# Kernel tuning notes

Hardware: AMD Instinct MI355X
Metric: run time of the kernel (lower is better)

## Reference

```python
import jax, jax.numpy as jnp
import numpy as np
from jax import lax

NUM_LAYERS = 4
D_MODEL = 768
D_STATE = 128
D_CONV = 4
EXPAND = 2
HEADDIM = 64
D_INNER = EXPAND * D_MODEL            # 1536
NHEADS = D_INNER // HEADDIM           # 24
NGROUPS = 1
CONV_DIM = D_INNER + 2 * NGROUPS * D_STATE        # 1792 (x, B, C go through conv)
D_PROJ = 2 * D_INNER + 2 * NGROUPS * D_STATE + NHEADS  # z, xBC, dt
BATCH, SEQ = 4, 2048


def silu(x):
    return x * jax.nn.sigmoid(x)


def rmsnorm(x, w, eps):
    xf = x.astype(jnp.float32)
    var = jnp.mean(xf * xf, axis=-1, keepdims=True)
    return (w * (xf * lax.rsqrt(var + eps)).astype(x.dtype))


def ssd_scan(xh, dt, A, B, C):
    # xh: (b,s,h,p)  dt: (b,s,h)  A: (h,)  B,C: (b,s,n)
    b = xh.shape[0]
    dA = jnp.exp(dt * A)  # (b,s,h)
    # time-major for scan
    dA_s = dA.transpose(1, 0, 2)          # (s,b,h)
    dt_s = dt.transpose(1, 0, 2)          # (s,b,h)
    x_s = xh.transpose(1, 0, 2, 3)        # (s,b,h,p)
    B_s = B.transpose(1, 0, 2)            # (s,b,n)
    C_s = C.transpose(1, 0, 2)            # (s,b,n)

    h0 = jnp.zeros((b, NHEADS, HEADDIM, D_STATE), xh.dtype)

    def step(h, inp):
        dA_t, dt_t, x_t, B_t, C_t = inp
        # h_t = exp(dt*A) * h_{t-1} + dt * x outer B
        dBx = (dt_t[:, :, None, None] * x_t[:, :, :, None]) * B_t[:, None, None, :]
        h = dA_t[:, :, None, None] * h + dBx
        y = jnp.einsum('bhpn,bn->bhp', h, C_t)
        return h, y

    _, ys = lax.scan(step, h0, (dA_s, dt_s, x_s, B_s, C_s))
    return ys.transpose(1, 0, 2, 3)  # (b,s,h,p)


def mamba2_block(x, Wi, cw, cb, dtb, Alog, Dp, gw, Wo):
    b, s, _ = x.shape
    zxbcdt = jnp.einsum('bsd,ed->bse', x, Wi)  # (b,s,D_PROJ)
    z = zxbcdt[..., :D_INNER]
    xBC = zxbcdt[..., D_INNER:D_INNER + CONV_DIM]
    dt = zxbcdt[..., D_INNER + CONV_DIM:]

    # causal depthwise conv over time on (x,B,C)
    xc = xBC.transpose(0, 2, 1)  # (b, conv_dim, s)
    xc = lax.conv_general_dilated(xc, cw[:, None, :], (1,), [(D_CONV - 1, 0)],
                                  feature_group_count=CONV_DIM)
    xc = xc + cb[None, :, None]
    xBC = silu(xc.transpose(0, 2, 1))

    x_ssm = xBC[..., :D_INNER]
    Bm = xBC[..., D_INNER:D_INNER + D_STATE]
    Cm = xBC[..., D_INNER + D_STATE:]

    dt = jax.nn.softplus(dt + dtb)           # (b,s,h)
    A = -jnp.exp(Alog)                       # (h,)
    xh = x_ssm.reshape(b, s, NHEADS, HEADDIM)

    y = ssd_scan(xh, dt, A, Bm, Cm) + Dp[None, None, :, None] * xh
    y = y.reshape(b, s, D_INNER)
    y = y * silu(z)                          # gated
    y = rmsnorm(y, gw, 1e-5)
    return jnp.einsum('bse,de->bsd', y, Wo)


def setup_inputs() -> dict:
    key = jax.random.key(0)
    ks = jax.random.split(key, 12)
    L = NUM_LAYERS
    sc_in = 1.0 / np.sqrt(D_MODEL)
    sc_out = 1.0 / np.sqrt(D_INNER)
    sc_conv = np.sqrt(2.0 / D_CONV)
    u = jax.random.uniform(ks[5], (L, NHEADS), minval=1e-3, maxval=0.1)
    return {
        'x': jax.random.normal(ks[0], (BATCH, SEQ, D_MODEL), jnp.float32),
        'in_proj_w': jax.random.normal(ks[1], (L, D_PROJ, D_MODEL), jnp.float32) * sc_in,
        'conv_w': jax.random.normal(ks[2], (L, CONV_DIM, D_CONV), jnp.float32) * sc_conv,
        'conv_b': jnp.zeros((L, CONV_DIM), jnp.float32),
        'dt_bias': jnp.log(jnp.expm1(u)),
        'A_log': jnp.log(jax.random.uniform(ks[6], (L, NHEADS), minval=1.0, maxval=16.0)),
        'D_skip': jnp.ones((L, NHEADS), jnp.float32),
        'gnorm_w': jnp.ones((L, D_INNER), jnp.float32),
        'out_proj_w': jax.random.normal(ks[7], (L, D_MODEL, D_INNER), jnp.float32) * sc_out,
        'ln_w': jnp.ones((L, D_MODEL), jnp.float32),
        'final_ln_w': jnp.ones((D_MODEL,), jnp.float32),
    }


def reference(x, in_proj_w, conv_w, conv_b, dt_bias, A_log, D_skip, gnorm_w,
              out_proj_w, ln_w, final_ln_w):
    for l in range(NUM_LAYERS):
        residual = x
        h = rmsnorm(x, ln_w[l], 1e-6)
        h = mamba2_block(h, in_proj_w[l], conv_w[l], conv_b[l], dt_bias[l],
                         A_log[l], D_skip[l], gnorm_w[l], out_proj_w[l])
        x = h + residual
    return rmsnorm(x, final_ln_w, 1e-6)
```

## Files before the change

kernel.cpp:

```cpp
#include <hip/hip_runtime.h>
#include <hip/hip_bf16.h>
#include <math.h>

#define NUM_LAYERS 4
#define D_MODEL 768
#define D_STATE 128
#define D_CONV 4
#define HEADDIM 64
#define D_INNER 1536
#define NHEADS 24
#define CONV_DIM 1792
#define D_PROJ 3352
#define BATCH 4
#define SEQ 2048
#define NROWS (BATCH*SEQ)
#define CHUNK 128
#define NCHUNK (SEQ/CHUNK)
#define LOG2E 1.4426950408889634f

typedef __bf16 bf16x8 __attribute__((ext_vector_type(8)));
typedef float f32x4 __attribute__((ext_vector_type(4)));

#define GLL(gsrc, ldst)                                                        \
  __builtin_amdgcn_global_load_lds(                                            \
      (const __attribute__((address_space(1))) unsigned int*)(gsrc),           \
      (__attribute__((address_space(3))) unsigned int*)(ldst), 16, 0, 0)

__device__ __forceinline__ float warp_reduce_sum(float v) {
  v += __shfl_xor(v, 32);
  v += __shfl_xor(v, 16);
  v += __shfl_xor(v, 8);
  v += __shfl_xor(v, 4);
  v += __shfl_xor(v, 2);
  v += __shfl_xor(v, 1);
  return v;
}

__device__ __forceinline__ float softplusf(float x) {
  return (x > 20.f) ? x : log1pf(expf(x));
}
__device__ __forceinline__ float siluf(float x) {
  return x / (1.f + expf(-x));
}

__device__ __forceinline__ void store_val(float v, float* p) { *p = v; }
__device__ __forceinline__ void store_val(float v, __hip_bfloat16* p) {
  *p = __float2bfloat16(v);
}

__global__ __launch_bounds__(256) void f32_to_bf16_kernel(
    const float* __restrict__ in, __hip_bfloat16* __restrict__ out, size_t n) {
  for (size_t i = ((size_t)blockIdx.x * 256 + threadIdx.x) * 4; i < n;
       i += (size_t)gridDim.x * 256 * 4) {
    float4 v = *(const float4*)(in + i);
    __hip_bfloat16 h0 = __float2bfloat16(v.x), h1 = __float2bfloat16(v.y);
    __hip_bfloat16 h2 = __float2bfloat16(v.z), h3 = __float2bfloat16(v.w);
    ushort4 u;
    u.x = *(unsigned short*)&h0; u.y = *(unsigned short*)&h1;
    u.z = *(unsigned short*)&h2; u.w = *(unsigned short*)&h3;
    *(ushort4*)(out + i) = u;
  }
}

template <typename OUT>
__global__ __launch_bounds__(256) void rmsnorm768_kernel(
    const float* __restrict__ in, const float* __restrict__ w,
    OUT* __restrict__ out, float eps) {
  int row = blockIdx.x;
  const float* x = in + (size_t)row * D_MODEL;
  OUT* o = out + (size_t)row * D_MODEL;
  int t = threadIdx.x;
  float v0 = x[t], v1 = x[t + 256], v2 = x[t + 512];
  float ss = v0 * v0 + v1 * v1 + v2 * v2;
  __shared__ float sred[4];
  ss = warp_reduce_sum(ss);
  if ((t & 63) == 0) sred[t >> 6] = ss;
  __syncthreads();
  float tot = sred[0] + sred[1] + sred[2] + sred[3];
  float inv = rsqrtf(tot / (float)D_MODEL + eps);
  store_val(w[t] * v0 * inv, o + t);
  store_val(w[t + 256] * v1 * inv, o + t + 256);
  store_val(w[t + 512] * v2 * inv, o + t + 512);
}

#define GEMM_PROLOGUE_AND_MAINLOOP(Asrc, Wsrc, Kdim)                           \
  int t = threadIdx.x;                                                         \
  int w = t >> 6, l = t & 63;                                                  \
  int NT = (Kdim) >> 5;                                                        \
  int ldsA0 = (w * 64) * 8;                                                    \
  int ldsA1 = (256 + w * 64) * 8;                                              \
  int lr = l & 15, lk = l >> 4;                                                \
  int wr = w >> 1, wc = w & 1;                                                 \
  int aoff = (lk * 128 + wr * 64 + lr) * 8;                                    \
  int boff = (lk * 128 + wc * 64 + lr) * 8;                                    \
  f32x4 acc[4][4];                                                             \
  _Pragma("unroll") for (int i = 0; i < 4; i++)                                \
      _Pragma("unroll") for (int j = 0; j < 4; j++) acc[i][j] = (f32x4)0.f;    \
  STAGE(0, 0);                                                                 \
  for (int kt = 0; kt < NT; ++kt) {                                            \
    int cur = kt & 1;                                                          \
    if (kt + 1 < NT) {                                                         \
      STAGE(cur ^ 1, (kt + 1) * 32);                                           \
      asm volatile("s_waitcnt vmcnt(4)" ::: "memory");                         \
    } else {                                                                   \
      asm volatile("s_waitcnt vmcnt(0)" ::: "memory");                         \
    }                                                                          \
    __builtin_amdgcn_sched_barrier(0);                                         \
    __builtin_amdgcn_s_barrier();                                              \
    __builtin_amdgcn_sched_barrier(0);                                         \
    bf16x8 av[4], bv[4];                                                       \
    _Pragma("unroll") for (int mi = 0; mi < 4; mi++)                           \
        av[mi] = *(const bf16x8*)&At[cur][aoff + mi * 128];                    \
    _Pragma("unroll") for (int ni = 0; ni < 4; ni++)                           \
        bv[ni] = *(const bf16x8*)&Bt[cur][boff + ni * 128];                    \
    _Pragma("unroll") for (int mi = 0; mi < 4; mi++)                           \
        _Pragma("unroll") for (int ni = 0; ni < 4; ni++)                       \
            acc[mi][ni] = __builtin_amdgcn_mfma_f32_16x16x32_bf16(             \
                av[mi], bv[ni], acc[mi][ni], 0, 0, 0);                         \
    __builtin_amdgcn_sched_barrier(0);                                         \
    __builtin_amdgcn_s_barrier();                                              \
  }

#define STAGE(buf, kofs)                                                       \
  do {                                                                         \
    GLL(Aptr + (kofs), &At[buf][ldsA0]);                                       \
    GLL(Aptr + (kofs) + 16, &At[buf][ldsA1]);                                  \
    GLL(Wptr + (kofs), &Bt[buf][ldsA0]);                                       \
    GLL(Wptr + (kofs) + 16, &Bt[buf][ldsA1]);                                  \
  } while (0)

__global__ __launch_bounds__(256) void gemm_bf16_kernel(
    const __hip_bfloat16* __restrict__ A, const __hip_bfloat16* __restrict__ W,
    const float* __restrict__ res, float* __restrict__ C,
    int M, int N, int K) {
  __shared__ __bf16 At[2][4096];
  __shared__ __bf16 Bt[2][4096];
  int cpx = gridDim.x >> 3;
  int bid = blockIdx.x;
  int bid2 = (bid & 7) * cpx + (bid >> 3);
  int nbn = (N + 127) >> 7;
  int bn = bid2 % nbn;
  int bm = bid2 / nbn;
  int m0 = bm * 128, n0 = bn * 128;
  int srow = threadIdx.x & 127;
  int kbase = (threadIdx.x >> 7) * 8;
  const __hip_bfloat16* Aptr = A + (size_t)(m0 + srow) * K + kbase;
  int nrow = n0 + srow; if (nrow >= N) nrow = N - 1;
  const __hip_bfloat16* Wptr = W + (size_t)nrow * K + kbase;

  GEMM_PROLOGUE_AND_MAINLOOP(A, W, K)

  int rbase = (l >> 4) * 4;
#pragma unroll
  for (int ni = 0; ni < 4; ni++) {
    int n = n0 + wc * 64 + ni * 16 + (l & 15);
    if (n >= N) continue;
#pragma unroll
    for (int mi = 0; mi < 4; mi++) {
#pragma unroll
      for (int r = 0; r < 4; r++) {
        int m = m0 + wr * 64 + mi * 16 + rbase + r;
        float v = acc[mi][ni][r];
        if (res) v += res[(size_t)m * N + n];
        C[(size_t)m * N + n] = v;
      }
    }
  }
}

__global__ __launch_bounds__(256) void gemm_inproj_kernel(
    const __hip_bfloat16* __restrict__ A, const __hip_bfloat16* __restrict__ W,
    __hip_bfloat16* __restrict__ zout, __hip_bfloat16* __restrict__ xout,
    float* __restrict__ dtout) {
  const int K = D_MODEL, N = D_PROJ;
  __shared__ __bf16 At[2][4096];
  __shared__ __bf16 Bt[2][4096];
  int cpx = gridDim.x >> 3;
  int bid = blockIdx.x;
  int bid2 = (bid & 7) * cpx + (bid >> 3);
  int bn = bid2 % 27;
  int bm = bid2 / 27;
  int m0 = bm * 128, n0 = bn * 128;
  int srow = threadIdx.x & 127;
  int kbase = (threadIdx.x >> 7) * 8;
  const __hip_bfloat16* Aptr = A + (size_t)(m0 + srow) * K + kbase;
  int nrow = n0 + srow; if (nrow >= N) nrow = N - 1;
  const __hip_bfloat16* Wptr = W + (size_t)nrow * K + kbase;

  GEMM_PROLOGUE_AND_MAINLOOP(A, W, K)

  int rbase = (l >> 4) * 4;
  if (bn < 12) {
#pragma unroll
    for (int ni = 0; ni < 4; ni++) {
      int n = n0 + wc * 64 + ni * 16 + (l & 15);
#pragma unroll
      for (int mi = 0; mi < 4; mi++)
#pragma unroll
        for (int r = 0; r < 4; r++) {
          int m = m0 + wr * 64 + mi * 16 + rbase + r;
          zout[(size_t)m * D_INNER + n] = __float2bfloat16(acc[mi][ni][r]);
        }
    }
  } else if (bn < 26) {
    int nb = n0 - D_INNER;
#pragma unroll
    for (int ni = 0; ni < 4; ni++) {
      int n = nb + wc * 64 + ni * 16 + (l & 15);
#pragma unroll
      for (int mi = 0; mi < 4; mi++)
#pragma unroll
        for (int r = 0; r < 4; r++) {
          int m = m0 + wr * 64 + mi * 16 + rbase + r;
          xout[(size_t)m * CONV_DIM + n] = __float2bfloat16(acc[mi][ni][r]);
        }
    }
  } else {
#pragma unroll
    for (int ni = 0; ni < 4; ni++) {
      int col = wc * 64 + ni * 16 + (l & 15);
      if (col >= 24) continue;
#pragma unroll
      for (int mi = 0; mi < 4; mi++)
#pragma unroll
        for (int r = 0; r < 4; r++) {
          int m = m0 + wr * 64 + mi * 16 + rbase + r;
          dtout[(size_t)m * 24 + col] = acc[mi][ni][r];
        }
    }
  }
}

__global__ __launch_bounds__(128) void dt_kernel(
    const float* __restrict__ dtraw, const float* __restrict__ dt_bias,
    const float* __restrict__ A_log, float* __restrict__ dtbuf,
    float* __restrict__ cum2buf) {
  int c = blockIdx.x & 15;
  int h = (blockIdx.x >> 4) % NHEADS;
  int b = blockIdx.x / (16 * NHEADS);
  int t = threadIdx.x;
  int s = c * CHUNK + t;
  float Ah = -expf(A_log[h]);
  float raw = dtraw[((size_t)b * SEQ + s) * 24 + h] + dt_bias[h];
  float dt = softplusf(raw);
  __shared__ float sc[128];
  sc[t] = dt * Ah;
  __syncthreads();
  for (int off = 1; off < 128; off <<= 1) {
    float v = (t >= off) ? sc[t - off] : 0.f;
    __syncthreads();
    sc[t] += v;
    __syncthreads();
  }
  size_t o = ((size_t)b * NHEADS + h) * SEQ + s;
  dtbuf[o] = dt;
  cum2buf[o] = sc[t] * LOG2E;
}

__global__ __launch_bounds__(256) void conv_tiles_kernel(
    const __hip_bfloat16* __restrict__ xbc, const float* __restrict__ cw,
    const float* __restrict__ cb, __hip_bfloat16* __restrict__ xA,
    __hip_bfloat16* __restrict__ Bkt, __hip_bfloat16* __restrict__ Bkn,
    __hip_bfloat16* __restrict__ Ckn) {
  __shared__ float srows[11 * CONV_DIM];
  int to = blockIdx.x & 15;
  int c  = (blockIdx.x >> 4) & 15;
  int b  = blockIdx.x >> 8;
  int t  = threadIdx.x;
  int sb = c * CHUNK + to * 8;
  const __hip_bfloat16* base = xbc + (size_t)b * SEQ * CONV_DIM;
  for (int e = t; e < 11 * 224; e += 256) {
    int r = e / 224, c8 = (e - r * 224) * 8;
    int s = sb - 3 + r;
    float* dst = &srows[r * CONV_DIM + c8];
    if (s >= 0) {
      bf16x8 v = *(const bf16x8*)&base[(size_t)s * CONV_DIM + c8];
#pragma unroll
      for (int j = 0; j < 8; j++) dst[j] = (float)v[j];
    } else {
#pragma unroll
      for (int j = 0; j < 8; j++) dst[j] = 0.f;
    }
  }
  __syncthreads();
  int bc = b * 16 + c;
#pragma unroll
  for (int k7 = 0; k7 < 7; k7++) {
    int ch = t + k7 * 256;
    float w0 = cw[ch * 4], w1 = cw[ch * 4 + 1];
    float w2 = cw[ch * 4 + 2], w3 = cw[ch * 4 + 3];
    float bias = cb[ch];
    float out[8];
#pragma unroll
    for (int j = 0; j < 8; j++) {
      float a = bias;
      a = fmaf(srows[(j + 0) * CONV_DIM + ch], w0, a);
      a = fmaf(srows[(j + 1) * CONV_DIM + ch], w1, a);
      a = fmaf(srows[(j + 2) * CONV_DIM + ch], w2, a);
      a = fmaf(srows[(j + 3) * CONV_DIM + ch], w3, a);
      out[j] = siluf(a);
    }
    if (ch < D_INNER) {
      int h = ch >> 6, p = ch & 63;
      bf16x8 v;
#pragma unroll
      for (int j = 0; j < 8; j++) v[j] = (__bf16)out[j];
      *(bf16x8*)&xA[((((size_t)bc * 24 + h) * 16 + to) * 64 + p) * 8] = v;
    } else if (ch < D_INNER + D_STATE) {
      int n = ch - D_INNER;
      bf16x8 v;
#pragma unroll
      for (int j = 0; j < 8; j++) v[j] = (__bf16)out[j];
      *(bf16x8*)&Bkt[(((size_t)bc * 16 + to) * 128 + n) * 8] = v;
      __hip_bfloat16* dst = Bkn + (size_t)bc * 16384 + ((n >> 3) * 128) * 8 + (n & 7);
#pragma unroll
      for (int j = 0; j < 8; j++)
        dst[(to * 8 + j) * 8] = __float2bfloat16(out[j]);
    } else {
      int n = ch - D_INNER - D_STATE;
      __hip_bfloat16* dst = Ckn + (size_t)bc * 16384 + ((n >> 3) * 128) * 8 + (n & 7);
#pragma unroll
      for (int j = 0; j < 8; j++)
        dst[(to * 8 + j) * 8] = __float2bfloat16(out[j]);
    }
  }
}

__global__ __launch_bounds__(256) void ssd_state_kernel(
    const __hip_bfloat16* __restrict__ xA, const __hip_bfloat16* __restrict__ Bkt,
    const float* __restrict__ dtbuf, const float* __restrict__ cum2buf,
    __hip_bfloat16* __restrict__ states) {
  __shared__ __bf16 sX[8192];
  __shared__ __bf16 sB[16384];
  __shared__ float swdt[128];
  int c = blockIdx.x & 15;
  int h = (blockIdx.x >> 4) % NHEADS;
  int b = blockIdx.x / (16 * NHEADS);
  int t = threadIdx.x;
  int l = t & 63, w = t >> 6;
  const __hip_bfloat16* xsrc = xA + ((size_t)(b * 16 + c) * 24 + h) * 8192;
  const __hip_bfloat16* bsrc = Bkt + (size_t)(b * 16 + c) * 16384;
#pragma unroll
  for (int i = 0; i < 4; i++) GLL(xsrc + (i * 256 + t) * 8, &sX[(i * 256 + t) * 8]);
#pragma unroll
  for (int i = 0; i < 8; i++) GLL(bsrc + (i * 256 + t) * 8, &sB[(i * 256 + t) * 8]);
  {
    size_t dto = ((size_t)b * NHEADS + h) * SEQ + c * CHUNK;
    if (t < 128) {
      float total2 = cum2buf[dto + 127];
      swdt[t] = dtbuf[dto + t] * exp2f(total2 - cum2buf[dto + t]);
    }
  }
  __syncthreads();
#pragma unroll
  for (int i = 0; i < 4; i++) {
    int o = i * 256 + t;
    int to = o >> 6;
    bf16x8 v = *(bf16x8*)&sX[o * 8];
#pragma unroll
    for (int j = 0; j < 8; j++)
      v[j] = (__bf16)((float)v[j] * swdt[to * 8 + j]);
    *(bf16x8*)&sX[o * 8] = v;
  }
  __syncthreads();
  int n0w = w * 32;
  f32x4 acc[4][2];
#pragma unroll
  for (int i = 0; i < 4; i++)
#pragma unroll
    for (int j = 0; j < 2; j++) acc[i][j] = (f32x4)0.f;
#pragma unroll
  for (int kk = 0; kk < 4; kk++) {
    int ko = kk * 4 + (l >> 4);
    bf16x8 av[4], bv[2];
#pragma unroll
    for (int mi = 0; mi < 4; mi++)
      av[mi] = *(const bf16x8*)&sX[(ko * 64 + mi * 16 + (l & 15)) * 8];
#pragma unroll
    for (int ni = 0; ni < 2; ni++)
      bv[ni] = *(const bf16x8*)&sB[(ko * 128 + n0w + ni * 16 + (l & 15)) * 8];
#pragma unroll
    for (int mi = 0; mi < 4; mi++)
#pragma unroll
      for (int ni = 0; ni < 2; ni++)
        acc[mi][ni] = __builtin_amdgcn_mfma_f32_16x16x32_bf16(
            av[mi], bv[ni], acc[mi][ni], 0, 0, 0);
  }
  __hip_bfloat16* dst = states + (((size_t)b * NHEADS + h) * 16 + c) * 8192;
#pragma unroll
  for (int mi = 0; mi < 4; mi++)
#pragma unroll
    for (int ni = 0; ni < 2; ni++) {
      int n = n0w + ni * 16 + (l & 15);
#pragma unroll
      for (int r = 0; r < 4; r++) {
        int p = mi * 16 + (l >> 4) * 4 + r;
        dst[((n >> 3) * 64 + p) * 8 + (n & 7)] = __float2bfloat16(acc[mi][ni][r]);
      }
    }
}

__global__ __launch_bounds__(256) void ssd_chunkscan_kernel(
    __hip_bfloat16* __restrict__ states, const float* __restrict__ cum2buf) {
  int q = blockIdx.x & 3;
  int bh = blockIdx.x >> 2;
  int t = threadIdx.x;
  int o = q * 256 + t;
  __hip_bfloat16* base = states + (size_t)bh * NCHUNK * 8192 + (size_t)o * 8;
  const float* c2 = cum2buf + (size_t)bh * SEQ;
  float hacc[8];
#pragma unroll
  for (int j = 0; j < 8; j++) hacc[j] = 0.f;
  for (int c = 0; c < NCHUNK; c++) {
    float eA = exp2f(c2[c * 128 + 127]);
    __hip_bfloat16* p = base + (size_t)c * 8192;
    bf16x8 v = *(bf16x8*)p;
    bf16x8 wv;
#pragma unroll
    for (int j = 0; j < 8; j++) {
      float tmp = (float)v[j];
      wv[j] = (__bf16)hacc[j];
      hacc[j] = fmaf(eA, hacc[j], tmp);
    }
    *(bf16x8*)p = wv;
  }
}

__global__ __launch_bounds__(256) void ssd_output_kernel(
    const __hip_bfloat16* __restrict__ Ckn, const __hip_bfloat16* __restrict__ Bkn,
    const __hip_bfloat16* __restrict__ xA, const __hip_bfloat16* __restrict__ states,
    const float* __restrict__ dtbuf, const float* __restrict__ cum2buf,
    const float* __restrict__ D_skip, __hip_bfloat16* __restrict__ y) {
  __shared__ __bf16 sC[16384];
  __shared__ __bf16 sBS[16384];
  __shared__ __bf16 sXH[8192];
  int c = blockIdx.x & 15;
  int h = (blockIdx.x >> 4) % NHEADS;
  int b = blockIdx.x / (16 * NHEADS);
  int t = threadIdx.x;
  int l = t & 63, w = t >> 6;
  int bc = b * 16 + c;
  const __hip_bfloat16* csrc = Ckn + (size_t)bc * 16384;
  const __hip_bfloat16* bsrc = Bkn + (size_t)bc * 16384;
  const __hip_bfloat16* xsrc = xA + ((size_t)bc * 24 + h) * 8192;
#pragma unroll
  for (int i = 0; i < 8; i++) GLL(csrc + (i * 256 + t) * 8, &sC[(i * 256 + t) * 8]);
#pragma unroll
  for (int i = 0; i < 8; i++) GLL(bsrc + (i * 256 + t) * 8, &sBS[(i * 256 + t) * 8]);
#pragma unroll
  for (int i = 0; i < 4; i++) GLL(xsrc + (i * 256 + t) * 8, &sXH[(i * 256 + t) * 8]);

  size_t dto = ((size_t)b * NHEADS + h) * SEQ + c * CHUNK;
  float cum2_t[8], cum2_tau[8], dt_tau[8];
#pragma unroll
  for (int fm = 0; fm < 2; fm++)
#pragma unroll
    for (int r = 0; r < 4; r++)
      cum2_t[fm * 4 + r] = cum2buf[dto + w * 32 + fm * 16 + (l >> 4) * 4 + r];
#pragma unroll
  for (int fc = 0; fc < 8; fc++) {
    cum2_tau[fc] = cum2buf[dto + fc * 16 + (l & 15)];
    dt_tau[fc] = dtbuf[dto + fc * 16 + (l & 15)];
  }
  float Dh = D_skip[h];
  __syncthreads();

  f32x4 g[2][8];
#pragma unroll
  for (int i = 0; i < 2; i++)
#pragma unroll
    for (int j = 0; j < 8; j++) g[i][j] = (f32x4)0.f;
#pragma unroll
  for (int kk = 0; kk < 4; kk++) {
    int ko = kk * 4 + (l >> 4);
    bf16x8 a0 = *(const bf16x8*)&sC[(ko * 128 + w * 32 + (l & 15)) * 8];
    bf16x8 a1 = *(const bf16x8*)&sC[(ko * 128 + w * 32 + 16 + (l & 15)) * 8];
#pragma unroll
    for (int fc = 0; fc < 8; fc++) {
      bf16x8 bv = *(const bf16x8*)&sBS[(ko * 128 + fc * 16 + (l & 15)) * 8];
      g[0][fc] = __builtin_amdgcn_mfma_f32_16x16x32_bf16(a0, bv, g[0][fc], 0, 0, 0);
      g[1][fc] = __builtin_amdgcn_mfma_f32_16x16x32_bf16(a1, bv, g[1][fc], 0, 0, 0);
    }
  }
  __syncthreads();

#pragma unroll
  for (int fm = 0; fm < 2; fm++)
#pragma unroll
    for (int fc = 0; fc < 8; fc++) {
      int tau = fc * 16 + (l & 15);
#pragma unroll
      for (int r = 0; r < 4; r++) {
        int tt = w * 32 + fm * 16 + (l >> 4) * 4 + r;
        float v = 0.f;
        if (tt >= tau) {
          v = exp2f(cum2_t[fm * 4 + r] - cum2_tau[fc]) * dt_tau[fc] * g[fm][fc][r];
          if (tt == tau) v += Dh;
        }
        sBS[((tau >> 3) * 128 + tt) * 8 + (tau & 7)] = (__bf16)v;
      }
    }
  f32x4 y1[2][4];
#pragma unroll
  for (int i = 0; i < 2; i++)
#pragma unroll
    for (int j = 0; j < 4; j++) y1[i][j] = (f32x4)0.f;
#pragma unroll
  for (int kk = 0; kk < 4; kk++) {
    int ko = kk * 4 + (l >> 4);
    bf16x8 a0 = *(const bf16x8*)&sBS[(ko * 128 + w * 32 + (l & 15)) * 8];
    bf16x8 a1 = *(const bf16x8*)&sBS[(ko * 128 + w * 32 + 16 + (l & 15)) * 8];
#pragma unroll
    for (int fc = 0; fc < 4; fc++) {
      bf16x8 bv = *(const bf16x8*)&sXH[(ko * 64 + fc * 16 + (l & 15)) * 8];
      y1[0][fc] = __builtin_amdgcn_mfma_f32_16x16x32_bf16(a0, bv, y1[0][fc], 0, 0, 0);
      y1[1][fc] = __builtin_amdgcn_mfma_f32_16x16x32_bf16(a1, bv, y1[1][fc], 0, 0, 0);
    }
  }
  __syncthreads();
  const __hip_bfloat16* hsrc = states + (((size_t)b * NHEADS + h) * 16 + c) * 8192;
#pragma unroll
  for (int i = 0; i < 4; i++) GLL(hsrc + (i * 256 + t) * 8, &sXH[(i * 256 + t) * 8]);
  __syncthreads();

  f32x4 y2[2][4];
#pragma unroll
  for (int i = 0; i < 2; i++)
#pragma unroll
    for (int j = 0; j < 4; j++) y2[i][j] = (f32x4)0.f;
#pragma unroll
  for (int kk = 0; kk < 4; kk++) {
    int ko = kk * 4 + (l >> 4);
    bf16x8 a0 = *(const bf16x8*)&sC[(ko * 128 + w * 32 + (l & 15)) * 8];
    bf16x8 a1 = *(const bf16x8*)&sC[(ko * 128 + w * 32 + 16 + (l & 15)) * 8];
#pragma unroll
    for (int fc = 0; fc < 4; fc++) {
      bf16x8 bv = *(const bf16x8*)&sXH[(ko * 64 + fc * 16 + (l & 15)) * 8];
      y2[0][fc] = __builtin_amdgcn_mfma_f32_16x16x32_bf16(a0, bv, y2[0][fc], 0, 0, 0);
      y2[1][fc] = __builtin_amdgcn_mfma_f32_16x16x32_bf16(a1, bv, y2[1][fc], 0, 0, 0);
    }
  }

  __hip_bfloat16* yr = y + ((size_t)b * SEQ + c * CHUNK) * D_INNER + h * 64;
#pragma unroll
  for (int fm = 0; fm < 2; fm++)
#pragma unroll
    for (int r = 0; r < 4; r++) {
      int tt = w * 32 + fm * 16 + (l >> 4) * 4 + r;
      float sdec = exp2f(cum2_t[fm * 4 + r]);
#pragma unroll
      for (int fc = 0; fc < 4; fc++) {
        int p = fc * 16 + (l & 15);
        yr[(size_t)tt * D_INNER + p] =
            __float2bfloat16(y1[fm][fc][r] + sdec * y2[fm][fc][r]);
      }
    }
}

__global__ __launch_bounds__(192) void gate_norm_kernel(
    __hip_bfloat16* __restrict__ y, const __hip_bfloat16* __restrict__ z,
    const float* __restrict__ gw) {
  int row = blockIdx.x;
  const __hip_bfloat16* zr = z + (size_t)row * D_INNER;
  __hip_bfloat16* yr = y + (size_t)row * D_INNER;
  int t = threadIdx.x;
  bf16x8 yv = *(const bf16x8*)&yr[t * 8];
  bf16x8 zv = *(const bf16x8*)&zr[t * 8];
  float vals[8];
  float ss = 0.f;
#pragma unroll
  for (int j = 0; j < 8; j++) {
    float zf = (float)zv[j];
    float v = (float)yv[j] * siluf(zf);
    vals[j] = v;
    ss += v * v;
  }
  __shared__ float sred[3];
  ss = warp_reduce_sum(ss);
  if ((t & 63) == 0) sred[t >> 6] = ss;
  __syncthreads();
  float tot = sred[0] + sred[1] + sred[2];
  float inv = rsqrtf(tot / (float)D_INNER + 1e-5f);
  bf16x8 o;
#pragma unroll
  for (int j = 0; j < 8; j++)
    o[j] = (__bf16)(gw[t * 8 + j] * vals[j] * inv);
  *(bf16x8*)&yr[t * 8] = o;
}

extern "C" void kernel_launch(void* const* d_in, const int* in_sizes, int n_in,
                              void* d_out, int out_size, void* d_ws, size_t ws_size,
                              hipStream_t stream) {
  const float* x          = (const float*)d_in[0];
  const float* in_proj_w  = (const float*)d_in[1];
  const float* conv_w     = (const float*)d_in[2];
  const float* conv_b     = (const float*)d_in[3];
  const float* dt_bias    = (const float*)d_in[4];
  const float* A_log      = (const float*)d_in[5];
  const float* D_skip     = (const float*)d_in[6];
  const float* gnorm_w    = (const float*)d_in[7];
  const float* out_proj_w = (const float*)d_in[8];
  const float* ln_w       = (const float*)d_in[9];
  const float* final_ln_w = (const float*)d_in[10];

  float* ws = (float*)d_ws;
  float* curx   = ws; ws += (size_t)NROWS * D_MODEL;
  float* dtraw  = ws; ws += (size_t)NROWS * 24;
  float* dtbuf  = ws; ws += (size_t)BATCH * NHEADS * SEQ;
  float* cum2   = ws; ws += (size_t)BATCH * NHEADS * SEQ;
  __hip_bfloat16* zbuf   = (__hip_bfloat16*)ws; ws += (size_t)NROWS * D_INNER / 2;
  __hip_bfloat16* xbcbuf = (__hip_bfloat16*)ws; ws += (size_t)NROWS * CONV_DIM / 2;
  __hip_bfloat16* hbuf_b = (__hip_bfloat16*)ws; ws += (size_t)NROWS * D_MODEL / 2;
  __hip_bfloat16* ybuf_b = (__hip_bfloat16*)ws; ws += (size_t)NROWS * D_INNER / 2;
  __hip_bfloat16* wi_b   = (__hip_bfloat16*)ws; ws += (size_t)NUM_LAYERS * D_PROJ * D_MODEL / 2;
  __hip_bfloat16* wo_b   = (__hip_bfloat16*)ws; ws += (size_t)NUM_LAYERS * D_MODEL * D_INNER / 2;
  __hip_bfloat16* xAb    = (__hip_bfloat16*)ws; ws += (size_t)BATCH * NCHUNK * 24 * 8192 / 2;
  __hip_bfloat16* Bkt    = (__hip_bfloat16*)ws; ws += (size_t)BATCH * NCHUNK * 16384 / 2;
  __hip_bfloat16* Bkn    = (__hip_bfloat16*)ws; ws += (size_t)BATCH * NCHUNK * 16384 / 2;
  __hip_bfloat16* Ckn    = (__hip_bfloat16*)ws; ws += (size_t)BATCH * NCHUNK * 16384 / 2;
  __hip_bfloat16* states = (__hip_bfloat16*)ws;

  f32_to_bf16_kernel<<<1024, 256, 0, stream>>>(
      in_proj_w, wi_b, (size_t)NUM_LAYERS * D_PROJ * D_MODEL);
  f32_to_bf16_kernel<<<1024, 256, 0, stream>>>(
      out_proj_w, wo_b, (size_t)NUM_LAYERS * D_MODEL * D_INNER);

  for (int l = 0; l < NUM_LAYERS; l++) {
    const float* xin = (l == 0) ? x : curx;
    rmsnorm768_kernel<__hip_bfloat16><<<NROWS, 256, 0, stream>>>(
        xin, ln_w + (size_t)l * D_MODEL, hbuf_b, 1e-6f);

    gemm_inproj_kernel<<<64 * 27, 256, 0, stream>>>(
        hbuf_b, wi_b + (size_t)l * D_PROJ * D_MODEL, zbuf, xbcbuf, dtraw);

    dt_kernel<<<BATCH * NHEADS * NCHUNK, 128, 0, stream>>>(
        dtraw, dt_bias + l * NHEADS, A_log + l * NHEADS, dtbuf, cum2);

    conv_tiles_kernel<<<BATCH * NCHUNK * 16, 256, 0, stream>>>(
        xbcbuf, conv_w + (size_t)l * CONV_DIM * D_CONV,
        conv_b + (size_t)l * CONV_DIM, xAb, Bkt, Bkn, Ckn);

    ssd_state_kernel<<<BATCH * NHEADS * NCHUNK, 256, 0, stream>>>(
        xAb, Bkt, dtbuf, cum2, states);

    ssd_chunkscan_kernel<<<BATCH * NHEADS * 4, 256, 0, stream>>>(states, cum2);

    ssd_output_kernel<<<BATCH * NHEADS * NCHUNK, 256, 0, stream>>>(
        Ckn, Bkn, xAb, states, dtbuf, cum2, D_skip + l * NHEADS, ybuf_b);

    gate_norm_kernel<<<NROWS, 192, 0, stream>>>(
        ybuf_b, zbuf, gnorm_w + (size_t)l * D_INNER);

    gemm_bf16_kernel<<<64 * 6, 256, 0, stream>>>(
        ybuf_b, wo_b + (size_t)l * D_MODEL * D_INNER, xin, curx,
        NROWS, D_MODEL, D_INNER);
  }
  rmsnorm768_kernel<float><<<NROWS, 256, 0, stream>>>(
      curx, final_ln_w, (float*)d_out, 1e-6f);
}
```

Baseline: 1.130 ms.

## Enlarge in-projection GEMM tile to 256x256 with 512 threads and set MFMA priority

Rewrites the in-projection GEMM to use 256x256 output tiles computed by 8 waves of 512 threads, with each wave owning a 128x64 sub-tile and double-buffered LDS staging. The larger tile raises arithmetic intensity and lowers redundant global loads of A and W. It also wraps the MFMA inner loops (including the shared GEMM macro) in s_setprio to favour matrix issue. The cost is more registers per thread, larger LDS use, and only 448 blocks, which may leave some compute units underused. The last N tile also wastes work because it covers only the 24 dt columns.

```diff
diff --git a/kernel.cpp b/kernel.cpp
--- a/kernel.cpp
+++ b/kernel.cpp
@@ -113,10 +113,12 @@
         av[mi] = *(const bf16x8*)&At[cur][aoff + mi * 128];                    \
     _Pragma("unroll") for (int ni = 0; ni < 4; ni++)                           \
         bv[ni] = *(const bf16x8*)&Bt[cur][boff + ni * 128];                    \
+    __builtin_amdgcn_s_setprio(1);                                             \
     _Pragma("unroll") for (int mi = 0; mi < 4; mi++)                           \
         _Pragma("unroll") for (int ni = 0; ni < 4; ni++)                       \
             acc[mi][ni] = __builtin_amdgcn_mfma_f32_16x16x32_bf16(             \
                 av[mi], bv[ni], acc[mi][ni], 0, 0, 0);                         \
+    __builtin_amdgcn_s_setprio(0);                                             \
     __builtin_amdgcn_sched_barrier(0);                                         \
     __builtin_amdgcn_s_barrier();                                              \
   }
@@ -168,64 +170,121 @@
   }
 }
 
-__global__ __launch_bounds__(256) void gemm_inproj_kernel(
+__global__ __launch_bounds__(512, 2) void gemm_inproj_kernel(
     const __hip_bfloat16* __restrict__ A, const __hip_bfloat16* __restrict__ W,
     __hip_bfloat16* __restrict__ zout, __hip_bfloat16* __restrict__ xout,
     float* __restrict__ dtout) {
   const int K = D_MODEL, N = D_PROJ;
-  __shared__ __bf16 At[2][4096];
-  __shared__ __bf16 Bt[2][4096];
+  __shared__ __bf16 At[2][8192];
+  __shared__ __bf16 Bt[2][8192];
   int cpx = gridDim.x >> 3;
   int bid = blockIdx.x;
   int bid2 = (bid & 7) * cpx + (bid >> 3);
-  int bn = bid2 % 27;
-  int bm = bid2 / 27;
-  int m0 = bm * 128, n0 = bn * 128;
-  int srow = threadIdx.x & 127;
-  int kbase = (threadIdx.x >> 7) * 8;
-  const __hip_bfloat16* Aptr = A + (size_t)(m0 + srow) * K + kbase;
-  int nrow = n0 + srow; if (nrow >= N) nrow = N - 1;
-  const __hip_bfloat16* Wptr = W + (size_t)nrow * K + kbase;
-
-  GEMM_PROLOGUE_AND_MAINLOOP(A, W, K)
+  int bn = bid2 % 14;
+  int bm = bid2 / 14;
+  int m0 = bm * 256, n0 = bn * 256;
+  int t = threadIdx.x;
+  int w = t >> 6, l = t & 63;
+
+  const __hip_bfloat16* Aptr[2];
+  const __hip_bfloat16* Wptr[2];
+  int dOff[2];
+#pragma unroll
+  for (int i = 0; i < 2; i++) {
+    int idx = i * 8 + w;
+    int oct = idx >> 2, rb = idx & 3;
+    dOff[i] = oct * 2048 + rb * 512;
+    Aptr[i] = A + (size_t)(m0 + rb * 64 + l) * K + oct * 8;
+    int wrow = n0 + rb * 64 + l; if (wrow >= N) wrow = N - 1;
+    Wptr[i] = W + (size_t)wrow * K + oct * 8;
+  }
+
+#define STAGE2(buf, kt)                                                        \
+  do {                                                                         \
+    _Pragma("unroll") for (int i = 0; i < 2; i++)                              \
+        GLL(Aptr[i] + (kt) * 32, &At[buf][dOff[i]]);                           \
+    _Pragma("unroll") for (int i = 0; i < 2; i++)                              \
+        GLL(Wptr[i] + (kt) * 32, &Bt[buf][dOff[i]]);                           \
+  } while (0)
+
+  int lr = l & 15, lk = l >> 4;
+  int wr = w >> 2, wc = w & 3;
+  f32x4 acc[8][4];
+#pragma unroll
+  for (int i = 0; i < 8; i++)
+#pragma unroll
+    for (int j = 0; j < 4; j++) acc[i][j] = (f32x4)0.f;
+
+  const int NT = 24;
+  STAGE2(0, 0);
+  for (int kt = 0; kt < NT; ++kt) {
+    int cur = kt & 1;
+    if (kt + 1 < NT) {
+      STAGE2(cur ^ 1, kt + 1);
+      asm volatile("s_waitcnt vmcnt(4)" ::: "memory");
+    } else {
+      asm volatile("s_waitcnt vmcnt(0)" ::: "memory");
+    }
+    __builtin_amdgcn_sched_barrier(0);
+    __builtin_amdgcn_s_barrier();
+    __builtin_amdgcn_sched_barrier(0);
+    bf16x8 av[8], bv[4];
+#pragma unroll
+    for (int mi = 0; mi < 8; mi++)
+      av[mi] = *(const bf16x8*)&At[cur][lk * 2048 + (wr * 128 + mi * 16 + lr) * 8];
+#pragma unroll
+    for (int ni = 0; ni < 4; ni++)
+      bv[ni] = *(const bf16x8*)&Bt[cur][lk * 2048 + (wc * 64 + ni * 16 + lr) * 8];
+    __builtin_amdgcn_s_setprio(1);
+#pragma unroll
+    for (int mi = 0; mi < 8; mi++)
+#pragma unroll
+      for (int ni = 0; ni < 4; ni++)
+        acc[mi][ni] = __builtin_amdgcn_mfma_f32_16x16x32_bf16(
+            av[mi], bv[ni], acc[mi][ni], 0, 0, 0);
+    __builtin_amdgcn_s_setprio(0);
+    __builtin_amdgcn_sched_barrier(0);
+    __builtin_amdgcn_s_barrier();
+  }
+#undef STAGE2
 
   int rbase = (l >> 4) * 4;
-  if (bn < 12) {
+  if (bn < 6) {
 #pragma unroll
     for (int ni = 0; ni < 4; ni++) {
-      int n = n0 + wc * 64 + ni * 16 + (l & 15);
-#pragma unroll
-      for (int mi = 0; mi < 4; mi++)
+      int n = n0 + wc * 64 + ni * 16 + lr;
+#pragma unroll
+      for (int mi = 0; mi < 8; mi++)
 #pragma unroll
         for (int r = 0; r < 4; r++) {
-          int m = m0 + wr * 64 + mi * 16 + rbase + r;
+          int m = m0 + wr * 128 + mi * 16 + rbase + r;
           zout[(size_t)m * D_INNER + n] = __float2bfloat16(acc[mi][ni][r]);
         }
     }
-  } else if (bn < 26) {
+  } else if (bn < 13) {
     int nb = n0 - D_INNER;
 #pragma unroll
     for (int ni = 0; ni < 4; ni++) {
-      int n = nb + wc * 64 + ni * 16 + (l & 15);
-#pragma unroll
-      for (int mi = 0; mi < 4; mi++)
+      int n = nb + wc * 64 + ni * 16 + lr;
+#pragma unroll
+      for (int mi = 0; mi < 8; mi++)
 #pragma unroll
         for (int r = 0; r < 4; r++) {
-          int m = m0 + wr * 64 + mi * 16 + rbase + r;
+          int m = m0 + wr * 128 + mi * 16 + rbase + r;
           xout[(size_t)m * CONV_DIM + n] = __float2bfloat16(acc[mi][ni][r]);
         }
     }
   } else {
 #pragma unroll
     for (int ni = 0; ni < 4; ni++) {
-      int col = wc * 64 + ni * 16 + (l & 15);
-      if (col >= 24) continue;
-#pragma unroll
-      for (int mi = 0; mi < 4; mi++)
+      int loc = wc * 64 + ni * 16 + lr;
+      if (loc >= 24) continue;
+#pragma unroll
+      for (int mi = 0; mi < 8; mi++)
 #pragma unroll
         for (int r = 0; r < 4; r++) {
-          int m = m0 + wr * 64 + mi * 16 + rbase + r;
-          dtout[(size_t)m * 24 + col] = acc[mi][ni][r];
+          int m = m0 + wr * 128 + mi * 16 + rbase + r;
+          dtout[(size_t)m * 24 + loc] = acc[mi][ni][r];
         }
     }
   }
@@ -630,7 +689,7 @@
     rmsnorm768_kernel<__hip_bfloat16><<<NROWS, 256, 0, stream>>>(
         xin, ln_w + (size_t)l * D_MODEL, hbuf_b, 1e-6f);
 
-    gemm_inproj_kernel<<<64 * 27, 256, 0, stream>>>(
+    gemm_inproj_kernel<<<448, 512, 0, stream>>>(
         hbuf_b, wi_b + (size_t)l * D_PROJ * D_MODEL, zbuf, xbcbuf, dtraw);
 
     dt_kernel<<<BATCH * NHEADS * NCHUNK, 128, 0, stream>>>(
```

Result: faster. 1.079 ms (-4.5%).
